# Optimization experiments

Measured on AMD Instinct MI355X. Metric: run time of the kernel, lower is better.

Reference implementation:

```python
import jax, jax.numpy as jnp
import numpy as np

EMBED_DIM = 128
FFN_DIM = 512
N_NODES = 50000
N_EDGES = 800000
LN_EPS = 1e-5


def setup_inputs() -> dict:
    key = jax.random.key(0)
    ks = jax.random.split(key, 8)
    s = 1.0 / np.sqrt(EMBED_DIM)
    return {
        "x": jax.random.normal(ks[0], (N_NODES, EMBED_DIM), jnp.float32),
        "edge_indices": jax.random.randint(ks[1], (2, N_EDGES), 0, N_NODES, dtype=jnp.int32),
        "W_qkv": jax.random.normal(ks[2], (EMBED_DIM, 3 * EMBED_DIM), jnp.float32) * s,
        "b_qkv": jnp.zeros((3 * EMBED_DIM,), jnp.float32),
        "W1": jax.random.normal(ks[3], (EMBED_DIM, FFN_DIM), jnp.float32) * s,
        "b1": jnp.zeros((FFN_DIM,), jnp.float32),
        "W2": jax.random.normal(ks[4], (FFN_DIM, EMBED_DIM), jnp.float32) * (1.0 / np.sqrt(FFN_DIM)),
        "b2": jnp.zeros((EMBED_DIM,), jnp.float32),
        "g1": jnp.ones((EMBED_DIM,), jnp.float32),
        "be1": jnp.zeros((EMBED_DIM,), jnp.float32),
        "g2": jnp.ones((EMBED_DIM,), jnp.float32),
        "be2": jnp.zeros((EMBED_DIM,), jnp.float32),
    }


def _layernorm(x, g, b):
    mu = jnp.mean(x, axis=-1, keepdims=True)
    var = jnp.mean(jnp.square(x - mu), axis=-1, keepdims=True)
    return (x - mu) * jax.lax.rsqrt(var + LN_EPS) * g + b


def _self_attention(x, edge_indices, W_qkv, b_qkv):
    n = x.shape[0]
    scale = x.shape[1] ** (-0.5)
    qkv = x @ W_qkv + b_qkv
    q, k, v = jnp.split(qkv, 3, axis=1)
    src, dst = edge_indices[0], edge_indices[1]  # row (softmax segment), col
    # per-edge logits: [E]
    alpha = jnp.sum(q[src] * k[dst], axis=1) * scale
    # segment (per-row) stable softmax
    m = jax.ops.segment_max(alpha, src, num_segments=n)
    e = jnp.exp(alpha - m[src])
    denom = jax.ops.segment_sum(e, src, num_segments=n)
    w = e / denom[src]  # [E]
    # sparse.mm: out[i] = sum_{(i,j) in E} w_ij * v[j]
    return jax.ops.segment_sum(w[:, None] * v[dst], src, num_segments=n)


def reference(x, edge_indices, W_qkv, b_qkv, W1, b1, W2, b2, g1, be1, g2, be2):
    # norm_first = False (post-norm), dropout = 0
    x = _layernorm(x + _self_attention(x, edge_indices, W_qkv, b_qkv), g1, be1)
    h = jax.nn.relu(x @ W1 + b1) @ W2 + b2
    x = _layernorm(x + h, g2, be2)
    return x
```

## Files before the change

kernel.cpp:

```cpp
#include <hip/hip_runtime.h>
#include <math.h>

#define NN 50000
#define NE 800000
#define ED 128
#define FD 512
#define MAXDEG 64
#define QKV_BLOCKS (NN / 16)
#define SCAT_BLOCKS ((NE + 255) / 256)
#define FFN_BLOCKS ((NN + 31) / 32)

typedef __attribute__((ext_vector_type(8))) short bf16x8;
typedef __attribute__((ext_vector_type(4))) float f32x4;
typedef _Float16 half2_t __attribute__((ext_vector_type(2)));

static __device__ __forceinline__ float wave_sum(float x) {
#pragma unroll
  for (int off = 32; off > 0; off >>= 1) x += __shfl_xor(x, off, 64);
  return x;
}

static __device__ __forceinline__ unsigned short f2bf(float f) {
  union { float f; unsigned u; } c; c.f = f;
  unsigned r = c.u + 0x7fffu + ((c.u >> 16) & 1u);
  return (unsigned short)(r >> 16);
}

static __device__ __forceinline__ unsigned short f2h(float f) {
  union { _Float16 h; unsigned short u; } c; c.h = (_Float16)f;
  return c.u;
}

static __device__ __forceinline__ half2_t u2h2(unsigned u) {
  union { unsigned u; half2_t h; } c; c.u = u;
  return c.h;
}

#if __has_builtin(__builtin_amdgcn_fdot2)
#define FDOT2(a, b, c) __builtin_amdgcn_fdot2((a), (b), (c), false)
#else
static __device__ __forceinline__ float FDOT2(half2_t a, half2_t b, float c) {
  return (float)a[0] * (float)b[0] + (float)a[1] * (float)b[1] + c;
}
#endif

__global__ void k_prep(const float* __restrict__ Wqkv, const float* __restrict__ W1,
                       const float* __restrict__ W2, unsigned short* __restrict__ WqkvF,
                       unsigned short* __restrict__ W1F, unsigned short* __restrict__ W2F,
                       int* __restrict__ cursor) {
  int idx = blockIdx.x * 256 + threadIdx.x;
  if (idx < NN) cursor[idx] = 0;
  if (idx < 49152) {
    int j = idx & 7, l = (idx >> 3) & 63, kb = (idx >> 9) & 3, t = idx >> 11;
    int k = kb * 32 + (l >> 4) * 8 + j, n = t * 16 + (l & 15);
    WqkvF[idx] = f2bf(Wqkv[k * 384 + n]);
  }
  {
    int j = idx & 7, l = (idx >> 3) & 63, kb = (idx >> 9) & 3, t = idx >> 11;
    int k = kb * 32 + (l >> 4) * 8 + j, n = t * 16 + (l & 15);
    W1F[idx] = f2bf(W1[k * 512 + n]);
  }
  {
    int j = idx & 7, l = (idx >> 3) & 63, kb = (idx >> 9) & 15, t = idx >> 13;
    int k = kb * 32 + (l >> 4) * 8 + j, n = t * 16 + (l & 15);
    W2F[idx] = f2bf(W2[k * 128 + n]);
  }
}

__global__ __launch_bounds__(256) void k_qkv_scat(
    const float* __restrict__ X, const unsigned short* __restrict__ WqkvF,
    const float* __restrict__ B, unsigned short* __restrict__ q,
    unsigned short* __restrict__ kv, const int* __restrict__ src,
    const int* __restrict__ dst, int* __restrict__ cursor,
    int* __restrict__ colidx) {
  __shared__ unsigned short xs[16][136];
  const int tid = threadIdx.x;
  if (blockIdx.x >= QKV_BLOCKS) {
    const int e = (blockIdx.x - QKV_BLOCKS) * 256 + tid;
    if (e < NE) {
      const int s = src[e];
      const int d = dst[e];
      const int slot = atomicAdd(&cursor[s], 1);
      if (slot < MAXDEG) colidx[s * MAXDEG + slot] = d;
    }
    return;
  }
  const int row0 = blockIdx.x * 16;
  for (int idx = tid; idx < 512; idx += 256) {
    int r = idx >> 5, c4 = (idx & 31) << 2;
    float4 val = *(const float4*)&X[(size_t)(row0 + r) * ED + c4];
    xs[r][c4] = f2bf(val.x); xs[r][c4 + 1] = f2bf(val.y);
    xs[r][c4 + 2] = f2bf(val.z); xs[r][c4 + 3] = f2bf(val.w);
  }
  __syncthreads();
  const int wv = tid >> 6, lane = tid & 63;
  const int ln = lane & 15, quad = lane >> 4;
  const int koff = quad * 8;
  bf16x8 a[4];
#pragma unroll
  for (int kb = 0; kb < 4; kb++) a[kb] = *(const bf16x8*)&xs[ln][kb * 32 + koff];
  for (int g = 0; g < 3; g++) {
    const int t0 = wv * 6 + g * 2;
    bf16x8 b[2][4];
#pragma unroll
    for (int j = 0; j < 2; j++)
#pragma unroll
      for (int kb = 0; kb < 4; kb++)
        b[j][kb] = *(const bf16x8*)&WqkvF[(size_t)(((t0 + j) * 4 + kb) * 64 + lane) * 8];
    f32x4 acc[2];
#pragma unroll
    for (int j = 0; j < 2; j++) acc[j] = (f32x4){0.f, 0.f, 0.f, 0.f};
#pragma unroll
    for (int kb = 0; kb < 4; kb++)
#pragma unroll
      for (int j = 0; j < 2; j++)
        acc[j] = __builtin_amdgcn_mfma_f32_16x16x32_bf16(a[kb], b[j][kb], acc[j], 0, 0, 0);
#pragma unroll
    for (int j = 0; j < 2; j++) {
      const int col = (t0 + j) * 16 + ln;
      const float bias = B[col];
      if (col < 128) {
#pragma unroll
        for (int r = 0; r < 4; r++)
          q[(size_t)(row0 + quad * 4 + r) * ED + col] =
              f2h((acc[j][r] + bias) * 0.08838834764831845f);
      } else {
#pragma unroll
        for (int r = 0; r < 4; r++)
          kv[(size_t)(row0 + quad * 4 + r) * 256 + (col - 128)] = f2h(acc[j][r] + bias);
      }
    }
  }
}

template <bool FULL>
static __device__ __forceinline__ void attn_chunk(
    int base, int cnt, int grp, int gl, int lane, const half2_t* qh,
    const unsigned short* __restrict__ kv, const int* __restrict__ colidx,
    float& l, half2_t* axh) {
  const int C = FULL ? 16 : cnt;
  int colreg = 0;
  if (lane < C) colreg = colidx[base + lane];
  const int itmax = FULL ? 4 : ((C + 3) >> 2);
#pragma unroll(FULL ? 4 : 1)
  for (int it = 0; it < itmax; it++) {
    const int t = it * 4 + grp;
    const bool act = FULL || t < C;
    const int cc = __shfl(colreg, act ? t : 0, 64);
    const unsigned short* row = &kv[(size_t)cc * 256 + gl * 8];
    uint4 kw = *(const uint4*)row;
    uint4 vw = *(const uint4*)(row + 128);
    float dot = FDOT2(qh[0], u2h2(kw.x), 0.f);
    dot = FDOT2(qh[1], u2h2(kw.y), dot);
    dot = FDOT2(qh[2], u2h2(kw.z), dot);
    dot = FDOT2(qh[3], u2h2(kw.w), dot);
    dot += __shfl_xor(dot, 1, 64);
    dot += __shfl_xor(dot, 2, 64);
    dot += __shfl_xor(dot, 4, 64);
    dot += __shfl_xor(dot, 8, 64);
    const float e = act ? __expf(dot) : 0.f;
    l += e;
    const half2_t e2 = {(_Float16)e, (_Float16)e};
    axh[0] += e2 * u2h2(vw.x);
    axh[1] += e2 * u2h2(vw.y);
    axh[2] += e2 * u2h2(vw.z);
    axh[3] += e2 * u2h2(vw.w);
  }
}

__global__ __launch_bounds__(256) void k_attn(
    const unsigned short* __restrict__ q, const unsigned short* __restrict__ kv,
    const float* __restrict__ x, const int* __restrict__ cursor,
    const int* __restrict__ colidx, unsigned short* __restrict__ attb) {
  const int wv = threadIdx.x >> 6;
  const int lane = threadIdx.x & 63;
  const int grp = lane >> 4, gl = lane & 15;
  const int node = blockIdx.x * 4 + wv;

  half2_t qh[4];
  {
    uint4 qw = *(const uint4*)&q[(size_t)node * ED + gl * 8];
    qh[0] = u2h2(qw.x); qh[1] = u2h2(qw.y);
    qh[2] = u2h2(qw.z); qh[3] = u2h2(qw.w);
  }
  const int cnt0 = cursor[node];
  const int cnt = cnt0 > MAXDEG ? MAXDEG : cnt0;
  const int b0 = node * MAXDEG;
  float l = 0.f;
  half2_t axh[4] = {};
  int off = 0;
  for (; off + 16 <= cnt; off += 16)
    attn_chunk<true>(b0 + off, 16, grp, gl, lane, qh, kv, colidx, l, axh);
  if (off < cnt)
    attn_chunk<false>(b0 + off, cnt - off, grp, gl, lane, qh, kv, colidx, l, axh);

#pragma unroll
  for (int j = 0; j < 4; j++) {
    union { half2_t h; int i; } c;
    union { int i; half2_t h; } d;
    c.h = axh[j]; d.i = __shfl_xor(c.i, 16, 64); axh[j] += d.h;
    c.h = axh[j]; d.i = __shfl_xor(c.i, 32, 64); axh[j] += d.h;
  }
  l += __shfl_xor(l, 16, 64);
  l += __shfl_xor(l, 32, 64);

  const float inv = (cnt > 0) ? 1.0f / l : 0.f;
  const int d0 = gl * 8 + grp * 2;
  const half2_t s = (grp == 0) ? axh[0] : (grp == 1) ? axh[1] : (grp == 2) ? axh[2] : axh[3];
  float2 xv = *(const float2*)&x[(size_t)node * ED + d0];
  unsigned pk = (unsigned)f2h(xv.x + (float)s[0] * inv) |
                ((unsigned)f2h(xv.y + (float)s[1] * inv) << 16);
  *(unsigned*)&attb[(size_t)node * ED + d0] = pk;
}

__global__ __launch_bounds__(256) void k_ffn_ln2(
    const unsigned short* __restrict__ attb, const unsigned short* __restrict__ W1F,
    const float* __restrict__ b1, const unsigned short* __restrict__ W2F,
    const float* __restrict__ b2, const float* __restrict__ g1,
    const float* __restrict__ be1, const float* __restrict__ g2,
    const float* __restrict__ be2, float* __restrict__ out) {
  __shared__ unsigned short xs[32][136];
  __shared__ unsigned short hs[32][520];
  __shared__ float ysf[32][132];
  float* ys = (float*)&hs[0][0];
  const int row0 = blockIdx.x * 32;
  const int tid = threadIdx.x;
  for (int i = tid; i < 512; i += 256) {
    const int r = i >> 4, c8 = (i & 15) << 3;
    const int row = row0 + r;
    if (row < NN) {
      uint4 aw = *(const uint4*)&attb[(size_t)row * ED + c8];
      half2_t h0 = u2h2(aw.x), h1 = u2h2(aw.y), h2 = u2h2(aw.z), h3 = u2h2(aw.w);
      ysf[r][c8] = (float)h0[0];     ysf[r][c8 + 1] = (float)h0[1];
      ysf[r][c8 + 2] = (float)h1[0]; ysf[r][c8 + 3] = (float)h1[1];
      ysf[r][c8 + 4] = (float)h2[0]; ysf[r][c8 + 5] = (float)h2[1];
      ysf[r][c8 + 6] = (float)h3[0]; ysf[r][c8 + 7] = (float)h3[1];
    } else {
#pragma unroll
      for (int k = 0; k < 8; k++) ysf[r][c8 + k] = 0.f;
    }
  }
  __syncthreads();
  const int wv = tid >> 6, lane = tid & 63;
#pragma unroll
  for (int pass = 0; pass < 4; pass++) {
    const int r = wv * 8 + pass * 2 + (lane >> 5);
    const int hd = (lane & 31) << 2;
    float4 vv = *(const float4*)&ysf[r][hd];
    float s4 = vv.x + vv.y + vv.z + vv.w;
#pragma unroll
    for (int off = 16; off > 0; off >>= 1) s4 += __shfl_xor(s4, off, 64);
    const float mean = s4 * (1.f / ED);
    const float dx0 = vv.x - mean, dx1 = vv.y - mean, dx2 = vv.z - mean, dx3 = vv.w - mean;
    float vr = dx0 * dx0 + dx1 * dx1 + dx2 * dx2 + dx3 * dx3;
#pragma unroll
    for (int off = 16; off > 0; off >>= 1) vr += __shfl_xor(vr, off, 64);
    const float rstd = rsqrtf(vr * (1.f / ED) + 1e-5f);
    const float4 gg = *(const float4*)&g1[hd];
    const float4 bb = *(const float4*)&be1[hd];
    const float o0 = dx0 * rstd * gg.x + bb.x;
    const float o1 = dx1 * rstd * gg.y + bb.y;
    const float o2 = dx2 * rstd * gg.z + bb.z;
    const float o3 = dx3 * rstd * gg.w + bb.w;
    xs[r][hd] = f2bf(o0); xs[r][hd + 1] = f2bf(o1);
    xs[r][hd + 2] = f2bf(o2); xs[r][hd + 3] = f2bf(o3);
    *(float4*)&ysf[r][hd] = make_float4(o0, o1, o2, o3);
  }
  __syncthreads();
  const int ln = lane & 15, quad = lane >> 4;
  const int koff = quad * 8;
  bf16x8 a1lo[4], a1hi[4];
#pragma unroll
  for (int kb = 0; kb < 4; kb++) {
    a1lo[kb] = *(const bf16x8*)&xs[ln][kb * 32 + koff];
    a1hi[kb] = *(const bf16x8*)&xs[16 + ln][kb * 32 + koff];
  }
  for (int g = 0; g < 4; g++) {
    const int t0 = wv * 8 + g * 2;
    bf16x8 b[2][4];
#pragma unroll
    for (int j = 0; j < 2; j++)
#pragma unroll
      for (int kb = 0; kb < 4; kb++)
        b[j][kb] = *(const bf16x8*)&W1F[(size_t)(((t0 + j) * 4 + kb) * 64 + lane) * 8];
    f32x4 acc[2][2];
#pragma unroll
    for (int j = 0; j < 2; j++)
#pragma unroll
      for (int h = 0; h < 2; h++) acc[j][h] = (f32x4){0.f, 0.f, 0.f, 0.f};
#pragma unroll
    for (int kb = 0; kb < 4; kb++)
#pragma unroll
      for (int j = 0; j < 2; j++) {
        acc[j][0] = __builtin_amdgcn_mfma_f32_16x16x32_bf16(a1lo[kb], b[j][kb], acc[j][0], 0, 0, 0);
        acc[j][1] = __builtin_amdgcn_mfma_f32_16x16x32_bf16(a1hi[kb], b[j][kb], acc[j][1], 0, 0, 0);
      }
#pragma unroll
    for (int j = 0; j < 2; j++) {
      const int col = (t0 + j) * 16 + ln;
      const float bias = b1[col];
#pragma unroll
      for (int r = 0; r < 4; r++) {
        hs[quad * 4 + r][col] = f2bf(fmaxf(acc[j][0][r] + bias, 0.f));
        hs[16 + quad * 4 + r][col] = f2bf(fmaxf(acc[j][1][r] + bias, 0.f));
      }
    }
  }
  __syncthreads();
  f32x4 acc2[2][2];
#pragma unroll
  for (int nt = 0; nt < 2; nt++)
#pragma unroll
    for (int h = 0; h < 2; h++) acc2[nt][h] = (f32x4){0.f, 0.f, 0.f, 0.f};
  const int nt0 = wv * 2;
  for (int kg = 0; kg < 4; kg++) {
    bf16x8 alo[4], ahi[4];
#pragma unroll
    for (int kk = 0; kk < 4; kk++) {
      alo[kk] = *(const bf16x8*)&hs[ln][(kg * 4 + kk) * 32 + koff];
      ahi[kk] = *(const bf16x8*)&hs[16 + ln][(kg * 4 + kk) * 32 + koff];
    }
    bf16x8 b[2][4];
#pragma unroll
    for (int nt = 0; nt < 2; nt++)
#pragma unroll
      for (int kk = 0; kk < 4; kk++)
        b[nt][kk] = *(const bf16x8*)&W2F[(size_t)(((nt0 + nt) * 16 + kg * 4 + kk) * 64 + lane) * 8];
#pragma unroll
    for (int kk = 0; kk < 4; kk++)
#pragma unroll
      for (int nt = 0; nt < 2; nt++) {
        acc2[nt][0] = __builtin_amdgcn_mfma_f32_16x16x32_bf16(alo[kk], b[nt][kk], acc2[nt][0], 0, 0, 0);
        acc2[nt][1] = __builtin_amdgcn_mfma_f32_16x16x32_bf16(ahi[kk], b[nt][kk], acc2[nt][1], 0, 0, 0);
      }
  }
  __syncthreads();
#pragma unroll
  for (int nt = 0; nt < 2; nt++) {
    const int col = (nt0 + nt) * 16 + ln;
    const float bias = b2[col];
#pragma unroll
    for (int r = 0; r < 4; r++) {
      ys[(quad * 4 + r) * 132 + col] = acc2[nt][0][r] + bias;
      ys[(16 + quad * 4 + r) * 132 + col] = acc2[nt][1][r] + bias;
    }
  }
  __syncthreads();
  float2 gg = *(const float2*)&g2[2 * lane];
  float2 bbe = *(const float2*)&be2[2 * lane];
#pragma unroll
  for (int rr = 0; rr < 8; rr++) {
    const int r = wv * 8 + rr;
    const int row = row0 + r;
    float vx = ys[r * 132 + 2 * lane] + ysf[r][2 * lane];
    float vy = ys[r * 132 + 2 * lane + 1] + ysf[r][2 * lane + 1];
    float mean = wave_sum(vx + vy) * (1.f / ED);
    float dx = vx - mean, dy = vy - mean;
    float var = wave_sum(dx * dx + dy * dy) * (1.f / ED);
    float rstd = rsqrtf(var + 1e-5f);
    if (row < NN) {
      float2 o = make_float2(dx * rstd * gg.x + bbe.x, dy * rstd * gg.y + bbe.y);
      *(float2*)&out[(size_t)row * ED + 2 * lane] = o;
    }
  }
}

extern "C" void kernel_launch(void* const* d_in, const int* in_sizes, int n_in,
                              void* d_out, int out_size, void* d_ws, size_t ws_size,
                              hipStream_t stream) {
  const float* x = (const float*)d_in[0];
  const int* ei = (const int*)d_in[1];
  const float* W_qkv = (const float*)d_in[2];
  const float* b_qkv = (const float*)d_in[3];
  const float* W1 = (const float*)d_in[4];
  const float* b1 = (const float*)d_in[5];
  const float* W2 = (const float*)d_in[6];
  const float* b2 = (const float*)d_in[7];
  const float* g1 = (const float*)d_in[8];
  const float* be1 = (const float*)d_in[9];
  const float* g2 = (const float*)d_in[10];
  const float* be2 = (const float*)d_in[11];
  float* out = (float*)d_out;

  char* ws = (char*)d_ws;
  size_t off = 0;
  auto alloc = [&](size_t bytes) -> char* {
    char* p = ws + off;
    off = (off + bytes + 255) & ~(size_t)255;
    return p;
  };
  unsigned short* q = (unsigned short*)alloc(2 * (size_t)NN * ED);
  unsigned short* kv = (unsigned short*)alloc(2 * (size_t)NN * 256);
  unsigned short* attb = (unsigned short*)alloc(2 * (size_t)NN * ED);
  unsigned short* WqkvF = (unsigned short*)alloc(2 * 24 * 4 * 64 * 8);
  unsigned short* W1F = (unsigned short*)alloc(2 * 32 * 4 * 64 * 8);
  unsigned short* W2F = (unsigned short*)alloc(2 * 8 * 16 * 64 * 8);
  int* cursor = (int*)alloc(sizeof(int) * NN);
  int* colidx = (int*)alloc(sizeof(int) * (size_t)NN * MAXDEG);

  k_prep<<<256, 256, 0, stream>>>(W_qkv, W1, W2, WqkvF, W1F, W2F, cursor);
  k_qkv_scat<<<QKV_BLOCKS + SCAT_BLOCKS, 256, 0, stream>>>(x, WqkvF, b_qkv, q, kv,
                                                           ei, ei + NE, cursor, colidx);
  k_attn<<<NN / 4, 256, 0, stream>>>(q, kv, x, cursor, colidx, attb);
  k_ffn_ln2<<<FFN_BLOCKS, 256, 0, stream>>>(attb, W1F, b1, W2F, b2, g1, be1, g2, be2, out);
}
```

Before: 279.1 us.

## Pad atomic cursors, use 16-bit colidx, interleave scatter blocks, halve FFN LDS

Each per-node atomic cursor now sits on its own cache-line-sized slot (stride 16 ints), to cut contention between atomics on neighbouring nodes. Neighbour column indices are stored as 16-bit values, which works because the node count is below 65536; this halves the adjacency traffic. QKV GEMM blocks and edge-scatter blocks are interleaved by block-index parity instead of running as two contiguous ranges, so both kinds of work are in flight together. The FFN kernel keeps its residual and LN1 buffer in fp16 rather than fp32, shrinking shared memory to allow more blocks per CU, at a small precision cost on the residual path.

```diff
diff --git a/kernel.cpp b/kernel.cpp
--- a/kernel.cpp
+++ b/kernel.cpp
@@ -6,6 +6,7 @@
 #define ED 128
 #define FD 512
 #define MAXDEG 64
+#define CURS_STRIDE 16
 #define QKV_BLOCKS (NN / 16)
 #define SCAT_BLOCKS ((NE + 255) / 256)
 #define FFN_BLOCKS ((NN + 31) / 32)
@@ -29,6 +30,11 @@
 static __device__ __forceinline__ unsigned short f2h(float f) {
   union { _Float16 h; unsigned short u; } c; c.h = (_Float16)f;
   return c.u;
+}
+
+static __device__ __forceinline__ float h2f(unsigned short u) {
+  union { unsigned short u; _Float16 h; } c; c.u = u;
+  return (float)c.h;
 }
 
 static __device__ __forceinline__ half2_t u2h2(unsigned u) {
@@ -49,7 +55,7 @@
                        unsigned short* __restrict__ W1F, unsigned short* __restrict__ W2F,
                        int* __restrict__ cursor) {
   int idx = blockIdx.x * 256 + threadIdx.x;
-  if (idx < NN) cursor[idx] = 0;
+  if (idx < NN) cursor[idx * CURS_STRIDE] = 0;
   if (idx < 49152) {
     int j = idx & 7, l = (idx >> 3) & 63, kb = (idx >> 9) & 3, t = idx >> 11;
     int k = kb * 32 + (l >> 4) * 8 + j, n = t * 16 + (l & 15);
@@ -72,20 +78,20 @@
     const float* __restrict__ B, unsigned short* __restrict__ q,
     unsigned short* __restrict__ kv, const int* __restrict__ src,
     const int* __restrict__ dst, int* __restrict__ cursor,
-    int* __restrict__ colidx) {
+    unsigned short* __restrict__ colidx) {
   __shared__ unsigned short xs[16][136];
   const int tid = threadIdx.x;
-  if (blockIdx.x >= QKV_BLOCKS) {
-    const int e = (blockIdx.x - QKV_BLOCKS) * 256 + tid;
+  if (blockIdx.x & 1) {
+    const int e = (blockIdx.x >> 1) * 256 + tid;
     if (e < NE) {
       const int s = src[e];
       const int d = dst[e];
-      const int slot = atomicAdd(&cursor[s], 1);
-      if (slot < MAXDEG) colidx[s * MAXDEG + slot] = d;
+      const int slot = atomicAdd(&cursor[s * CURS_STRIDE], 1);
+      if (slot < MAXDEG) colidx[s * MAXDEG + slot] = (unsigned short)d;
     }
     return;
   }
-  const int row0 = blockIdx.x * 16;
+  const int row0 = (blockIdx.x >> 1) * 16;
   for (int idx = tid; idx < 512; idx += 256) {
     int r = idx >> 5, c4 = (idx & 31) << 2;
     float4 val = *(const float4*)&X[(size_t)(row0 + r) * ED + c4];
@@ -136,7 +142,7 @@
 template <bool FULL>
 static __device__ __forceinline__ void attn_chunk(
     int base, int cnt, int grp, int gl, int lane, const half2_t* qh,
-    const unsigned short* __restrict__ kv, const int* __restrict__ colidx,
+    const unsigned short* __restrict__ kv, const unsigned short* __restrict__ colidx,
     float& l, half2_t* axh) {
   const int C = FULL ? 16 : cnt;
   int colreg = 0;
@@ -171,7 +177,7 @@
 __global__ __launch_bounds__(256) void k_attn(
     const unsigned short* __restrict__ q, const unsigned short* __restrict__ kv,
     const float* __restrict__ x, const int* __restrict__ cursor,
-    const int* __restrict__ colidx, unsigned short* __restrict__ attb) {
+    const unsigned short* __restrict__ colidx, unsigned short* __restrict__ attb) {
   const int wv = threadIdx.x >> 6;
   const int lane = threadIdx.x & 63;
   const int grp = lane >> 4, gl = lane & 15;
@@ -183,7 +189,7 @@
     qh[0] = u2h2(qw.x); qh[1] = u2h2(qw.y);
     qh[2] = u2h2(qw.z); qh[3] = u2h2(qw.w);
   }
-  const int cnt0 = cursor[node];
+  const int cnt0 = cursor[node * CURS_STRIDE];
   const int cnt = cnt0 > MAXDEG ? MAXDEG : cnt0;
   const int b0 = node * MAXDEG;
   float l = 0.f;
@@ -221,24 +227,17 @@
     const float* __restrict__ be2, float* __restrict__ out) {
   __shared__ unsigned short xs[32][136];
   __shared__ unsigned short hs[32][520];
-  __shared__ float ysf[32][132];
+  __shared__ unsigned short ysf[32][136];
   float* ys = (float*)&hs[0][0];
   const int row0 = blockIdx.x * 32;
   const int tid = threadIdx.x;
   for (int i = tid; i < 512; i += 256) {
     const int r = i >> 4, c8 = (i & 15) << 3;
     const int row = row0 + r;
-    if (row < NN) {
-      uint4 aw = *(const uint4*)&attb[(size_t)row * ED + c8];
-      half2_t h0 = u2h2(aw.x), h1 = u2h2(aw.y), h2 = u2h2(aw.z), h3 = u2h2(aw.w);
-      ysf[r][c8] = (float)h0[0];     ysf[r][c8 + 1] = (float)h0[1];
-      ysf[r][c8 + 2] = (float)h1[0]; ysf[r][c8 + 3] = (float)h1[1];
-      ysf[r][c8 + 4] = (float)h2[0]; ysf[r][c8 + 5] = (float)h2[1];
-      ysf[r][c8 + 6] = (float)h3[0]; ysf[r][c8 + 7] = (float)h3[1];
-    } else {
-#pragma unroll
-      for (int k = 0; k < 8; k++) ysf[r][c8 + k] = 0.f;
-    }
+    uint4 aw = (row < NN) ? *(const uint4*)&attb[(size_t)row * ED + c8]
+                          : make_uint4(0, 0, 0, 0);
+    *(uint2*)&ysf[r][c8] = make_uint2(aw.x, aw.y);
+    *(uint2*)&ysf[r][c8 + 4] = make_uint2(aw.z, aw.w);
   }
   __syncthreads();
   const int wv = tid >> 6, lane = tid & 63;
@@ -246,12 +245,14 @@
   for (int pass = 0; pass < 4; pass++) {
     const int r = wv * 8 + pass * 2 + (lane >> 5);
     const int hd = (lane & 31) << 2;
-    float4 vv = *(const float4*)&ysf[r][hd];
-    float s4 = vv.x + vv.y + vv.z + vv.w;
+    uint2 pv = *(const uint2*)&ysf[r][hd];
+    half2_t a01 = u2h2(pv.x), a23 = u2h2(pv.y);
+    float v0 = (float)a01[0], v1 = (float)a01[1], v2 = (float)a23[0], v3 = (float)a23[1];
+    float s4 = v0 + v1 + v2 + v3;
 #pragma unroll
     for (int off = 16; off > 0; off >>= 1) s4 += __shfl_xor(s4, off, 64);
     const float mean = s4 * (1.f / ED);
-    const float dx0 = vv.x - mean, dx1 = vv.y - mean, dx2 = vv.z - mean, dx3 = vv.w - mean;
+    const float dx0 = v0 - mean, dx1 = v1 - mean, dx2 = v2 - mean, dx3 = v3 - mean;
     float vr = dx0 * dx0 + dx1 * dx1 + dx2 * dx2 + dx3 * dx3;
 #pragma unroll
     for (int off = 16; off > 0; off >>= 1) vr += __shfl_xor(vr, off, 64);
@@ -264,7 +265,8 @@
     const float o3 = dx3 * rstd * gg.w + bb.w;
     xs[r][hd] = f2bf(o0); xs[r][hd + 1] = f2bf(o1);
     xs[r][hd + 2] = f2bf(o2); xs[r][hd + 3] = f2bf(o3);
-    *(float4*)&ysf[r][hd] = make_float4(o0, o1, o2, o3);
+    ysf[r][hd] = f2h(o0); ysf[r][hd + 1] = f2h(o1);
+    ysf[r][hd + 2] = f2h(o2); ysf[r][hd + 3] = f2h(o3);
   }
   __syncthreads();
   const int ln = lane & 15, quad = lane >> 4;
@@ -352,8 +354,8 @@
   for (int rr = 0; rr < 8; rr++) {
     const int r = wv * 8 + rr;
     const int row = row0 + r;
-    float vx = ys[r * 132 + 2 * lane] + ysf[r][2 * lane];
-    float vy = ys[r * 132 + 2 * lane + 1] + ysf[r][2 * lane + 1];
+    float vx = ys[r * 132 + 2 * lane] + h2f(ysf[r][2 * lane]);
+    float vy = ys[r * 132 + 2 * lane + 1] + h2f(ysf[r][2 * lane + 1]);
     float mean = wave_sum(vx + vy) * (1.f / ED);
     float dx = vx - mean, dy = vy - mean;
     float var = wave_sum(dx * dx + dy * dy) * (1.f / ED);
@@ -395,8 +397,8 @@
   unsigned short* WqkvF = (unsigned short*)alloc(2 * 24 * 4 * 64 * 8);
   unsigned short* W1F = (unsigned short*)alloc(2 * 32 * 4 * 64 * 8);
   unsigned short* W2F = (unsigned short*)alloc(2 * 8 * 16 * 64 * 8);
-  int* cursor = (int*)alloc(sizeof(int) * NN);
-  int* colidx = (int*)alloc(sizeof(int) * (size_t)NN * MAXDEG);
+  int* cursor = (int*)alloc(sizeof(int) * (size_t)NN * CURS_STRIDE);
+  unsigned short* colidx = (unsigned short*)alloc(sizeof(unsigned short) * (size_t)NN * MAXDEG);
 
   k_prep<<<256, 256, 0, stream>>>(W_qkv, W1, W2, WqkvF, W1F, W2F, cursor);
   k_qkv_scat<<<QKV_BLOCKS + SCAT_BLOCKS, 256, 0, stream>>>(x, WqkvF, b_qkv, q, kv,
```

After: 245.6 us. 1.14x faster.
